# Optimization experiments

Measured on AMD Instinct MI355X. Metric: run time of the kernel, lower is better.

## Reference

```python
import jax, jax.numpy as jnp
import numpy as np

# dims from source: seq_len=784, d_in=2, d_hidden=512, d_out=2, n_layers=3; batch bumped 32->64
T, BS, D_IN, D_H, D_OUT, N_LAYERS = 784, 64, 2, 512, 2, 3


def _glorot(k, shape):
    fan_in, fan_out = shape[-2], shape[-1]
    std = jnp.sqrt(2.0 / (fan_in + fan_out)).astype(jnp.float32)
    return jax.random.normal(k, shape, jnp.float32) * std


def setup_inputs() -> dict:
    key = jax.random.key(0)
    ks = jax.random.split(key, 8)
    x = jax.random.normal(ks[0], (T, BS, D_IN), jnp.float32)
    W0 = _glorot(ks[1], (D_IN, D_H))
    b0 = jnp.zeros((D_H,), jnp.float32)
    # stable_init: uniform in [0.999, 1.001), one diagonal 'a' per layer
    A = jax.random.uniform(ks[2], (N_LAYERS, D_H), jnp.float32, 0.999, 1.001)
    B = _glorot(ks[3], (N_LAYERS, D_H, D_H))  # per-layer input matrix b
    C = _glorot(ks[4], (N_LAYERS, D_H, D_H))  # per-layer output matrix c
    Wf = _glorot(ks[5], (D_H, D_OUT))
    bf = jnp.zeros((D_OUT,), jnp.float32)
    return {"x": x, "W0": W0, "b0": b0, "A": A, "B": B, "C": C, "Wf": Wf, "bf": bf}


def _rnn_layer(x, a, b, c):
    # x: [T, BS, D], diagonal linear recurrence h_t = h_{t-1} * a + x_t @ b; y_t = h_t @ c
    u = jnp.einsum('tbi,ih->tbh', x, b)  # batched GEMM outside the scan

    def step(h, u_t):
        h = h * a + u_t
        return h, h

    h0 = jnp.zeros(u.shape[1:], u.dtype)  # [BS, D_H]
    _, hs = jax.lax.scan(step, h0, u)     # hs: [T, BS, D_H]
    return jnp.einsum('tbh,ho->tbo', hs, c)


def reference(x, W0, b0, A, B, C, Wf, bf):
    # initial Dense + relu
    h = jax.nn.relu(x @ W0 + b0)
    # stacked unidirectional RNN layers, relu after each
    for l in range(A.shape[0]):
        h = jax.nn.relu(_rnn_layer(h, A[l], B[l], C[l]))
    # final Dense (no residual)
    return h @ Wf + bf
```

## Files before the change

kernel.cpp:

```cpp
#include <hip/hip_runtime.h>
#include <hip/hip_bf16.h>

typedef _Float16 f16;
typedef f16 f16x8 __attribute__((ext_vector_type(8)));
typedef float f32x4 __attribute__((ext_vector_type(4)));

#define T_LEN 784
#define BATCH 64
#define DH 512
#define NCH (BATCH*DH)
#define M_ROWS (T_LEN*BATCH)
#define NCHUNK 16
#define CLEN 49

#define ACT_SCALE (1.0f/256.0f)
#define ACT_INV   256.0f

#define GLL16(g, s)                                                             \
    __builtin_amdgcn_global_load_lds(                                           \
        (const __attribute__((address_space(1))) void*)(g),                     \
        (__attribute__((address_space(3))) void*)(s), 16, 0, 0)

__global__ void prep_weights(const float* __restrict__ B, const float* __restrict__ C,
                             f16* __restrict__ Bt, f16* __restrict__ Ct) {
    __shared__ float tile[32][33];
    int z = blockIdx.z;
    const float* src = (z < 3) ? (B + (size_t)z * DH * DH) : (C + (size_t)(z - 3) * DH * DH);
    f16* dst = (z < 3) ? (Bt + (size_t)z * DH * DH) : (Ct + (size_t)(z - 3) * DH * DH);
    int tx = threadIdx.x, ty = threadIdx.y;
    int nb = blockIdx.x * 32, kb = blockIdx.y * 32;
#pragma unroll
    for (int i = 0; i < 4; i++) {
        int k = ty + i * 8;
        tile[k][tx] = src[(size_t)(kb + k) * DH + nb + tx];
    }
    __syncthreads();
#pragma unroll
    for (int i = 0; i < 4; i++) {
        int n = ty + i * 8;
        dst[(size_t)(nb + n) * DH + kb + tx] = (f16)tile[tx][n];
    }
}

__global__ void dense0_kernel(const float* __restrict__ x, const float* __restrict__ W0,
                              const float* __restrict__ b0, f16* __restrict__ H) {
    int tid = blockIdx.x * 256 + threadIdx.x;
    int m = tid >> 6;
    int hb = (tid & 63) * 8;
    float x0 = x[(size_t)m * 2], x1 = x[(size_t)m * 2 + 1];
    f32x4 wa0 = *(const f32x4*)(W0 + hb);
    f32x4 wa1 = *(const f32x4*)(W0 + hb + 4);
    f32x4 wb0 = *(const f32x4*)(W0 + DH + hb);
    f32x4 wb1 = *(const f32x4*)(W0 + DH + hb + 4);
    f32x4 c0 = *(const f32x4*)(b0 + hb);
    f32x4 c1 = *(const f32x4*)(b0 + hb + 4);
    f16x8 o;
#pragma unroll
    for (int j = 0; j < 4; j++) {
        float v = fmaxf(fmaf(x0, wa0[j], fmaf(x1, wb0[j], c0[j])), 0.f) * ACT_SCALE;
        o[j] = (f16)v;
    }
#pragma unroll
    for (int j = 0; j < 4; j++) {
        float v = fmaxf(fmaf(x0, wa1[j], fmaf(x1, wb1[j], c1[j])), 0.f) * ACT_SCALE;
        o[4 + j] = (f16)v;
    }
    *(f16x8*)(H + (size_t)m * DH + hb) = o;
}

template <int RELU>
__global__ __launch_bounds__(256) void gemm_k(const f16* __restrict__ A,
                                              const f16* __restrict__ Bt,
                                              f16* __restrict__ Out) {
    __shared__ __align__(16) f16 As[2][128 * 32];
    __shared__ __align__(16) f16 Bs[2][128 * 32];
    const int tid = threadIdx.x;
    const int lane = tid & 63;
    const int wave = tid >> 6;
    const int wr = wave >> 1, wc = wave & 1;
    const size_t mb = (size_t)blockIdx.x * 128;
    const int nb = blockIdx.y * 128;

    const int rl = lane >> 2, sl = lane & 3;
    const int ssl = sl ^ ((rl >> 1) & 3);
    const int rowS0 = wave * 16 + rl;
    const int rowS1 = 64 + wave * 16 + rl;
    const f16* gA0 = A + (mb + rowS0) * DH + ssl * 8;
    const f16* gA1 = A + (mb + rowS1) * DH + ssl * 8;
    const f16* gB0 = Bt + (size_t)(nb + rowS0) * DH + ssl * 8;
    const f16* gB1 = Bt + (size_t)(nb + rowS1) * DH + ssl * 8;
    const int ldsOff0 = (wave * 16) * 32;
    const int ldsOff1 = (64 + wave * 16) * 32;

    const int rA = lane & 15, kq = lane >> 4;
    const int fsl = kq ^ ((rA >> 1) & 3);
    int offA[4], offB[4];
#pragma unroll
    for (int i = 0; i < 4; i++) offA[i] = (wr * 64 + i * 16 + rA) * 32 + fsl * 8;
#pragma unroll
    for (int j = 0; j < 4; j++) offB[j] = (wc * 64 + j * 16 + rA) * 32 + fsl * 8;

    f32x4 acc[4][4] = {};

#define STAGE(b, kt)                        \
    do {                                    \
        GLL16(gA0 + (kt), &As[b][ldsOff0]); \
        GLL16(gA1 + (kt), &As[b][ldsOff1]); \
        GLL16(gB0 + (kt), &Bs[b][ldsOff0]); \
        GLL16(gB1 + (kt), &Bs[b][ldsOff1]); \
    } while (0)

    STAGE(0, 0);
    __syncthreads();
    int buf = 0;
    for (int t = 0; t < 15; ++t) {
        STAGE(buf ^ 1, (t + 1) * 32);
        f16x8 af[4], bg[4];
#pragma unroll
        for (int i = 0; i < 4; i++) af[i] = *(const f16x8*)&As[buf][offA[i]];
#pragma unroll
        for (int j = 0; j < 4; j++) bg[j] = *(const f16x8*)&Bs[buf][offB[j]];
#pragma unroll
        for (int i = 0; i < 4; i++)
#pragma unroll
            for (int j = 0; j < 4; j++)
                acc[i][j] = __builtin_amdgcn_mfma_f32_16x16x32_f16(af[i], bg[j], acc[i][j], 0, 0, 0);
        __syncthreads();
        buf ^= 1;
    }
    {
        f16x8 af[4], bg[4];
#pragma unroll
        for (int i = 0; i < 4; i++) af[i] = *(const f16x8*)&As[buf][offA[i]];
#pragma unroll
        for (int j = 0; j < 4; j++) bg[j] = *(const f16x8*)&Bs[buf][offB[j]];
#pragma unroll
        for (int i = 0; i < 4; i++)
#pragma unroll
            for (int j = 0; j < 4; j++)
                acc[i][j] = __builtin_amdgcn_mfma_f32_16x16x32_f16(af[i], bg[j], acc[i][j], 0, 0, 0);
    }
#undef STAGE

    const int crow = (lane >> 4) * 4;
    const int ccol = lane & 15;
#pragma unroll
    for (int i = 0; i < 4; i++)
#pragma unroll
        for (int j = 0; j < 4; j++) {
#pragma unroll
            for (int r = 0; r < 4; r++) {
                size_t row = mb + wr * 64 + i * 16 + crow + r;
                int col = nb + wc * 64 + j * 16 + ccol;
                float v = acc[i][j][r];
                if (RELU) v = fmaxf(v, 0.f);
                Out[row * DH + col] = (f16)v;
            }
        }
}

__global__ void scan_pass1(const f16* __restrict__ U, const float* __restrict__ Al,
                           float* __restrict__ finals) {
    int tid = blockIdx.x * 256 + threadIdx.x;
    int ch = tid & (NCH - 1);
    int c = tid >> 15;
    float a = Al[ch & (DH - 1)];
    const f16* p = U + (size_t)(c * CLEN) * NCH + ch;
    float h = 0.f;
#pragma unroll
    for (int i = 0; i < CLEN; i++) h = fmaf(h, a, (float)p[(size_t)i * NCH]);
    finals[(size_t)c * NCH + ch] = h;
}

__global__ void scan_pass2(const float* __restrict__ finals, const float* __restrict__ Al,
                           float* __restrict__ carries) {
    int ch = blockIdx.x * 256 + threadIdx.x;
    float a = Al[ch & (DH - 1)];
    float a49 = 1.f;
#pragma unroll
    for (int i = 0; i < CLEN; i++) a49 *= a;
    float carry = 0.f;
#pragma unroll
    for (int c = 0; c < NCHUNK; c++) {
        carries[(size_t)c * NCH + ch] = carry;
        carry = fmaf(carry, a49, finals[(size_t)c * NCH + ch]);
    }
}

__global__ void scan_pass3(f16* __restrict__ U, const float* __restrict__ Al,
                           const float* __restrict__ carries) {
    int tid = blockIdx.x * 256 + threadIdx.x;
    int ch = tid & (NCH - 1);
    int c = tid >> 15;
    float a = Al[ch & (DH - 1)];
    f16* p = U + (size_t)(c * CLEN) * NCH + ch;
    float h = carries[(size_t)c * NCH + ch];
#pragma unroll
    for (int i = 0; i < CLEN; i++) {
        h = fmaf(h, a, (float)p[(size_t)i * NCH]);
        p[(size_t)i * NCH] = (f16)h;
    }
}

__global__ void final_dense(const f16* __restrict__ H, const float* __restrict__ Wf,
                            const float* __restrict__ bf_, float* __restrict__ out) {
    __shared__ float WfS[DH * 2];
    for (int i = threadIdx.x; i < DH * 2; i += 256) WfS[i] = Wf[i];
    __syncthreads();
    int wave = threadIdx.x >> 6, lane = threadIdx.x & 63;
    size_t m = (size_t)blockIdx.x * 4 + wave;
    f16x8 v = *(const f16x8*)(H + m * DH + lane * 8);
    float d0 = 0.f, d1 = 0.f;
#pragma unroll
    for (int j = 0; j < 8; j++) {
        float hv = (float)v[j];
        int h = lane * 8 + j;
        d0 = fmaf(hv, WfS[h * 2], d0);
        d1 = fmaf(hv, WfS[h * 2 + 1], d1);
    }
#pragma unroll
    for (int off = 32; off; off >>= 1) {
        d0 += __shfl_down(d0, off);
        d1 += __shfl_down(d1, off);
    }
    if (lane == 0) {
        out[m * 2] = fmaf(d0, ACT_INV, bf_[0]);
        out[m * 2 + 1] = fmaf(d1, ACT_INV, bf_[1]);
    }
}

extern "C" void kernel_launch(void* const* d_in, const int* in_sizes, int n_in,
                              void* d_out, int out_size, void* d_ws, size_t ws_size,
                              hipStream_t stream) {
    (void)in_sizes; (void)n_in; (void)out_size; (void)ws_size;
    const float* x   = (const float*)d_in[0];
    const float* W0  = (const float*)d_in[1];
    const float* b0  = (const float*)d_in[2];
    const float* A   = (const float*)d_in[3];
    const float* Bw  = (const float*)d_in[4];
    const float* Cw  = (const float*)d_in[5];
    const float* Wf  = (const float*)d_in[6];
    const float* bfv = (const float*)d_in[7];
    float* out = (float*)d_out;

    char* ws = (char*)d_ws;
    size_t off = 0;
    auto alloc = [&](size_t bytes) {
        void* p = ws + off;
        off += (bytes + 255) & ~(size_t)255;
        return p;
    };
    f16* Bt = (f16*)alloc((size_t)3 * DH * DH * 2);
    f16* Ct = (f16*)alloc((size_t)3 * DH * DH * 2);
    f16* P  = (f16*)alloc((size_t)M_ROWS * DH * 2);
    f16* Q  = (f16*)alloc((size_t)M_ROWS * DH * 2);
    float* finals  = (float*)alloc((size_t)NCH * NCHUNK * 4);
    float* carries = (float*)alloc((size_t)NCH * NCHUNK * 4);

    dim3 b256(256);
    prep_weights<<<dim3(16, 16, 6), dim3(32, 8), 0, stream>>>(Bw, Cw, Bt, Ct);
    dense0_kernel<<<M_ROWS * 64 / 256, b256, 0, stream>>>(x, W0, b0, P);
    for (int l = 0; l < 3; l++) {
        const float* Al = A + l * DH;
        gemm_k<0><<<dim3(M_ROWS / 128, 4), b256, 0, stream>>>(P, Bt + (size_t)l * DH * DH, Q);
        scan_pass1<<<NCH * NCHUNK / 256, b256, 0, stream>>>(Q, Al, finals);
        scan_pass2<<<NCH / 256, b256, 0, stream>>>(finals, Al, carries);
        scan_pass3<<<NCH * NCHUNK / 256, b256, 0, stream>>>(Q, Al, carries);
        gemm_k<1><<<dim3(M_ROWS / 128, 4), b256, 0, stream>>>(Q, Ct + (size_t)l * DH * DH, P);
    }
    final_dense<<<M_ROWS / 4, b256, 0, stream>>>(P, Wf, bfv, out);
}
```

Before: 380.5 us.

## Deepen GEMM LDS pipeline to four stages with explicit vmcnt waits

The GEMM main loop changes from a double-buffered LDS scheme with a full __syncthreads per k-step to a four-buffer ring. Three tiles are prefetched and the kernel waits with s_waitcnt vmcnt on only the oldest outstanding loads before a bare barrier. This keeps more global-to-LDS loads in flight and removes full drains, to hide memory latency. LDS use doubles to 64KB per block, which may reduce occupancy, and correctness now relies on the manual vmcnt counts.

```diff
diff --git a/kernel.cpp b/kernel.cpp
--- a/kernel.cpp
+++ b/kernel.cpp
@@ -20,6 +20,8 @@
     __builtin_amdgcn_global_load_lds(                                           \
         (const __attribute__((address_space(1))) void*)(g),                     \
         (__attribute__((address_space(3))) void*)(s), 16, 0, 0)
+
+#define VMCNT(n) asm volatile("s_waitcnt vmcnt(" #n ")" ::: "memory")
 
 __global__ void prep_weights(const float* __restrict__ B, const float* __restrict__ C,
                              f16* __restrict__ Bt, f16* __restrict__ Ct) {
@@ -72,8 +74,8 @@
 __global__ __launch_bounds__(256) void gemm_k(const f16* __restrict__ A,
                                               const f16* __restrict__ Bt,
                                               f16* __restrict__ Out) {
-    __shared__ __align__(16) f16 As[2][128 * 32];
-    __shared__ __align__(16) f16 Bs[2][128 * 32];
+    __shared__ __align__(16) f16 As[4][128 * 32];
+    __shared__ __align__(16) f16 Bs[4][128 * 32];
     const int tid = threadIdx.x;
     const int lane = tid & 63;
     const int wave = tid >> 6;
@@ -110,37 +112,37 @@
         GLL16(gB1 + (kt), &Bs[b][ldsOff1]); \
     } while (0)
 
+#define COMPUTE(b)                                                                              \
+    do {                                                                                        \
+        f16x8 af[4], bg[4];                                                                     \
+        _Pragma("unroll") for (int i = 0; i < 4; i++) af[i] = *(const f16x8*)&As[b][offA[i]];   \
+        _Pragma("unroll") for (int j = 0; j < 4; j++) bg[j] = *(const f16x8*)&Bs[b][offB[j]];   \
+        _Pragma("unroll") for (int i = 0; i < 4; i++)                                           \
+        _Pragma("unroll") for (int j = 0; j < 4; j++)                                           \
+            acc[i][j] = __builtin_amdgcn_mfma_f32_16x16x32_f16(af[i], bg[j], acc[i][j], 0, 0, 0); \
+    } while (0)
+
     STAGE(0, 0);
-    __syncthreads();
-    int buf = 0;
-    for (int t = 0; t < 15; ++t) {
-        STAGE(buf ^ 1, (t + 1) * 32);
-        f16x8 af[4], bg[4];
-#pragma unroll
-        for (int i = 0; i < 4; i++) af[i] = *(const f16x8*)&As[buf][offA[i]];
-#pragma unroll
-        for (int j = 0; j < 4; j++) bg[j] = *(const f16x8*)&Bs[buf][offB[j]];
-#pragma unroll
-        for (int i = 0; i < 4; i++)
-#pragma unroll
-            for (int j = 0; j < 4; j++)
-                acc[i][j] = __builtin_amdgcn_mfma_f32_16x16x32_f16(af[i], bg[j], acc[i][j], 0, 0, 0);
-        __syncthreads();
-        buf ^= 1;
-    }
-    {
-        f16x8 af[4], bg[4];
-#pragma unroll
-        for (int i = 0; i < 4; i++) af[i] = *(const f16x8*)&As[buf][offA[i]];
-#pragma unroll
-        for (int j = 0; j < 4; j++) bg[j] = *(const f16x8*)&Bs[buf][offB[j]];
-#pragma unroll
-        for (int i = 0; i < 4; i++)
-#pragma unroll
-            for (int j = 0; j < 4; j++)
-                acc[i][j] = __builtin_amdgcn_mfma_f32_16x16x32_f16(af[i], bg[j], acc[i][j], 0, 0, 0);
-    }
+    STAGE(1, 32);
+    STAGE(2, 64);
+
+    for (int t = 0; t < 13; ++t) {
+        VMCNT(8);
+        __builtin_amdgcn_s_barrier();
+        STAGE((t + 3) & 3, (t + 3) * 32);
+        COMPUTE(t & 3);
+    }
+    VMCNT(8);
+    __builtin_amdgcn_s_barrier();
+    COMPUTE(1);
+    VMCNT(4);
+    __builtin_amdgcn_s_barrier();
+    COMPUTE(2);
+    VMCNT(0);
+    __builtin_amdgcn_s_barrier();
+    COMPUTE(3);
 #undef STAGE
+#undef COMPUTE
 
     const int crow = (lane >> 4) * 4;
     const int ccol = lane & 15;
```

After: 450.2 us. 1.18x slower.
